# Optimization experiments

Hardware: AMD Instinct MI355X
Metric: run time of the kernel (lower is better)

Reference implementation:

```python
import jax, jax.numpy as jnp
import numpy as np

B, D_IN, D_FEAT = 256, 512, 512   # batch, encoder in-dim, encoder out-dim (= Sender input_dim)
H, V, E, L = 512, 32000, 64, 16   # hidden_size, vocab_size, embedding_dim, length


def setup_inputs() -> dict:
    key = jax.random.key(0)
    ks = jax.random.split(key, 12)
    s = lambda *d: 1.0 / np.sqrt(d[-1])
    return {
        "x": jax.random.normal(ks[0], (B, D_IN), jnp.float32),
        # encoder: Linear(D_IN, D_FEAT)
        "enc_W": jax.random.normal(ks[1], (D_FEAT, D_IN), jnp.float32) * s(D_IN),
        "enc_b": jnp.zeros((D_FEAT,), jnp.float32),
        # input_layer: Linear(D_FEAT, H)
        "in_W": jax.random.normal(ks[2], (H, D_FEAT), jnp.float32) * s(D_FEAT),
        "in_b": jnp.zeros((H,), jnp.float32),
        # GRU cell (torch layout: gates ordered r, z, n)
        "W_ih": jax.random.normal(ks[3], (3 * H, E), jnp.float32) * s(H),
        "W_hh": jax.random.normal(ks[4], (3 * H, H), jnp.float32) * s(H),
        "b_ih": jnp.zeros((3 * H,), jnp.float32),
        "b_hh": jnp.zeros((3 * H,), jnp.float32),
        # output_layer: Linear(H, V)
        "out_W": jax.random.normal(ks[5], (V, H), jnp.float32) * s(H),
        "out_b": jnp.zeros((V,), jnp.float32),
        # msg_embedding table and sos embedding parameter
        "emb_table": jax.random.normal(ks[6], (V, E), jnp.float32),
        "sos_emb": jax.random.normal(ks[7], (E,), jnp.float32),
    }


def _gru_cell(e, h, W_ih, W_hh, b_ih, b_hh):
    gi = e @ W_ih.T + b_ih            # [B, 3H]
    gh = h @ W_hh.T + b_hh            # [B, 3H]
    gi_r, gi_z, gi_n = jnp.split(gi, 3, axis=-1)
    gh_r, gh_z, gh_n = jnp.split(gh, 3, axis=-1)
    r = jax.nn.sigmoid(gi_r + gh_r)
    z = jax.nn.sigmoid(gi_z + gh_z)
    n = jnp.tanh(gi_n + r * gh_n)
    return (1.0 - z) * n + z * h


def reference(x, enc_W, enc_b, in_W, in_b, W_ih, W_hh, b_ih, b_hh,
              out_W, out_b, emb_table, sos_emb):
    # encoder -> input_layer -> initial hidden state (num_layers = 1)
    feat = x @ enc_W.T + enc_b                  # [B, D_FEAT]
    h0 = feat @ in_W.T + in_b                   # [B, H]
    e0 = jnp.broadcast_to(sos_emb, (x.shape[0], E))  # sos embedding repeated over batch

    def step(carry, _):
        h, e = carry
        h = _gru_cell(e, h, W_ih, W_hh, b_ih, b_hh)      # [B, H]
        logits_t = h @ out_W.T + out_b                    # [B, V]
        sym = jnp.argmax(logits_t, axis=-1)               # eval-mode greedy symbol [B]
        e_next = emb_table[sym]                           # [B, E]
        return (h, e_next), (sym, logits_t)

    (_, _), (syms, logits) = jax.lax.scan(step, (h0, e0), None, length=L)
    sequence = syms.T                                     # [B, L] int
    logits = jnp.transpose(logits, (1, 0, 2))             # [B, L, V]
    return sequence, logits
```

## Files before the change

### kernel.cpp

```cpp
#include <hip/hip_runtime.h>
#include <math.h>

#define BATCH 256
#define DIN 512
#define DFEAT 512
#define HSZ 512
#define VOCAB 32000
#define EMB 64
#define SLEN 16
#define NTILE 500
#define MARGIN 0.0625f

typedef __attribute__((ext_vector_type(8))) short bf16x8;
typedef __attribute__((ext_vector_type(4))) float f32x4;

__device__ inline unsigned bf16_rne(float x) {
    union { float f; unsigned u; } u; u.f = x;
    unsigned r = u.u + 0x7fff + ((u.u >> 16) & 1);
    return r >> 16;
}

template<int BM, int BN, int BK, int TM, int TN>
__global__ __launch_bounds__(256) void gemm_atb(
    const float* __restrict__ A,
    const float* __restrict__ W,
    const float* __restrict__ bias,
    float* __restrict__ C, long long ldc,
    int M, int N, int K)
{
    __shared__ float As[BK][BM + 4];
    __shared__ float Bs[BK][BN + 4];
    constexpr int THREADS = (BM / TM) * (BN / TN);
    const int tid = threadIdx.x;
    const int tx = tid % (BN / TN);
    const int ty = tid / (BN / TN);
    const int row0 = blockIdx.y * BM;
    const int col0 = blockIdx.x * BN;
    float acc[TM][TN] = {};
    for (int k0 = 0; k0 < K; k0 += BK) {
        for (int i = tid; i < BM * BK; i += THREADS) {
            int m = i / BK, k = i % BK;
            As[k][m] = A[(long long)(row0 + m) * K + k0 + k];
        }
        for (int i = tid; i < BN * BK; i += THREADS) {
            int n = i / BK, k = i % BK;
            Bs[k][n] = W[(long long)(col0 + n) * K + k0 + k];
        }
        __syncthreads();
        #pragma unroll
        for (int kk = 0; kk < BK; ++kk) {
            float a[TM], b[TN];
            #pragma unroll
            for (int i = 0; i < TM; ++i) a[i] = As[kk][ty * TM + i];
            #pragma unroll
            for (int j = 0; j < TN; ++j) b[j] = Bs[kk][tx * TN + j];
            #pragma unroll
            for (int i = 0; i < TM; ++i)
                #pragma unroll
                for (int j = 0; j < TN; ++j)
                    acc[i][j] = fmaf(a[i], b[j], acc[i][j]);
        }
        __syncthreads();
    }
    #pragma unroll
    for (int i = 0; i < TM; ++i) {
        long long m = row0 + ty * TM + i;
        float* crow = C + m * ldc;
        #pragma unroll
        for (int j = 0; j < TN; ++j) {
            int n = col0 + tx * TN + j;
            float v = acc[i][j];
            if (bias) v += bias[n];
            crow[n] = v;
        }
    }
}

__global__ void prep_kernel(const float* __restrict__ out_W, ushort* __restrict__ Wb,
                            const float* __restrict__ W_ih, const float* __restrict__ W_hh,
                            const float* __restrict__ b_ih, const float* __restrict__ b_hh,
                            float* __restrict__ Wcat2, float* __restrict__ bcat2)
{
    const int stride = gridDim.x * 256;
    const int t0 = blockIdx.x * 256 + threadIdx.x;
    for (int i = t0; i < VOCAB * HSZ / 4; i += stride) {
        const float4 v = ((const float4*)out_W)[i];
        ushort4 o;
        o.x = (ushort)bf16_rne(v.x); o.y = (ushort)bf16_rne(v.y);
        o.z = (ushort)bf16_rne(v.z); o.w = (ushort)bf16_rne(v.w);
        ((ushort4*)Wb)[i] = o;
    }
    for (long long i = t0; i < 2048LL * 576; i += stride) {
        int g = (int)(i / 576), k = (int)(i % 576);
        int j = g >> 2, comp = g & 3;
        float v;
        if (comp == 0)      v = (k < 64) ? W_ih[j * 64 + k]          : W_hh[(long long)j * 512 + k - 64];
        else if (comp == 1) v = (k < 64) ? W_ih[(512 + j) * 64 + k]  : W_hh[(long long)(512 + j) * 512 + k - 64];
        else if (comp == 2) v = (k < 64) ? W_ih[(1024 + j) * 64 + k] : 0.f;
        else                v = (k < 64) ? 0.f                        : W_hh[(long long)(1024 + j) * 512 + k - 64];
        Wcat2[i] = v;
    }
    for (int i = t0; i < 2048; i += stride) {
        int j = i >> 2, comp = i & 3;
        float bv = (comp == 0) ? b_ih[j] + b_hh[j]
                 : (comp == 1) ? b_ih[512 + j] + b_hh[512 + j]
                 : (comp == 2) ? b_ih[1024 + j] : b_hh[1024 + j];
        bcat2[i] = bv;
    }
}

template<bool FIRST>
__global__ __launch_bounds__(256) void gru_fused_kernel(
    const float* __restrict__ hprev, float* __restrict__ hnew,
    const float* __restrict__ Wcat2, const float* __restrict__ bcat2,
    const float* __restrict__ ebuf, const float* __restrict__ sos,
    ushort* __restrict__ hbf)
{
    __shared__ __align__(16) char smem[22528];
    const int tid = threadIdx.x;
    const int blk = blockIdx.x;
    const int ty = blk >> 5;
    const int tx = blk & 31;
    float* As = (float*)smem;
    float* Bs = (float*)(smem + 4608);
    const int tyt = tid >> 4;
    const int txt = tid & 15;
    float acc[4] = {};
    for (int k0 = 0; k0 < 576; k0 += 64) {
        for (int i = tid; i < 16 * 64; i += 256) {
            int m = i >> 6, k = i & 63;
            int kc = k0 + k;
            float v;
            if (kc < 64) v = FIRST ? sos[kc] : ebuf[(long long)(ty * 16 + m) * 64 + kc];
            else         v = hprev[(long long)(ty * 16 + m) * 512 + kc - 64];
            As[k * 18 + m] = v;
        }
        for (int i = tid; i < 64 * 64; i += 256) {
            int n = i >> 6, k = i & 63;
            Bs[k * 68 + n] = Wcat2[(long long)(tx * 64 + n) * 576 + k0 + k];
        }
        __syncthreads();
        #pragma unroll 8
        for (int kk = 0; kk < 64; ++kk) {
            const float a = As[kk * 18 + tyt];
            const float4 b = *(const float4*)&Bs[kk * 68 + txt * 4];
            acc[0] = fmaf(a, b.x, acc[0]);
            acc[1] = fmaf(a, b.y, acc[1]);
            acc[2] = fmaf(a, b.z, acc[2]);
            acc[3] = fmaf(a, b.w, acc[3]);
        }
        __syncthreads();
    }
    float* gt = (float*)smem;
    #pragma unroll
    for (int j = 0; j < 4; ++j)
        gt[tyt * 64 + txt * 4 + j] = acc[j];
    __syncthreads();
    {
        int row = tid >> 4, jl = tid & 15;
        int jg = tx * 16 + jl;
        float gr  = gt[row * 64 + jl * 4 + 0] + bcat2[jg * 4 + 0];
        float gz  = gt[row * 64 + jl * 4 + 1] + bcat2[jg * 4 + 1];
        float gni = gt[row * 64 + jl * 4 + 2] + bcat2[jg * 4 + 2];
        float gnh = gt[row * 64 + jl * 4 + 3] + bcat2[jg * 4 + 3];
        float r = 1.0f / (1.0f + expf(-gr));
        float z = 1.0f / (1.0f + expf(-gz));
        float n = tanhf(gni + r * gnh);
        long long bglob = ty * 16 + row;
        float hold = hprev[bglob * 512 + jg];
        float h = (1.0f - z) * n + z * hold;
        hnew[bglob * 512 + jg] = h;
        hbf[bglob * 512 + jg] = (ushort)bf16_rne(h);
    }
}

__global__ __launch_bounds__(256) void logits_bm128_kernel(
    const ushort* __restrict__ hbf,
    const ushort* __restrict__ Wb,
    const float* __restrict__ out_b,
    float* __restrict__ lbase, float* __restrict__ tmaxv)
{
    __shared__ __align__(16) char As[16384];
    __shared__ __align__(16) char Bs[8192];
    __shared__ float s_mv[128];
    const int tid = threadIdx.x;
    const int lane = tid & 63;
    const int wave = tid >> 6;
    const int bid = blockIdx.x;
    const int job = (bid & 7) * 125 + (bid >> 3);
    const int jx = job >> 1;
    const int jy = job & 1;
    const int row0 = jy * 128;
    const int col0 = jx * 64;

    f32x4 acc[2][4] = {};
    const int srow = tid >> 3;
    const int sch = tid & 7;

    for (int k0 = 0; k0 < 512; k0 += 64) {
        #pragma unroll
        for (int ra = 0; ra < 4; ++ra) {
            int row = ra * 32 + srow;
            const char* g = (const char*)(hbf + (long long)(row0 + row) * 512 + k0) + ((sch ^ (row & 7)) * 16);
            __builtin_amdgcn_global_load_lds(
                (const __attribute__((address_space(1))) void*)g,
                (__attribute__((address_space(3))) void*)(As + row * 128 + sch * 16), 16, 0, 0);
        }
        #pragma unroll
        for (int rb = 0; rb < 2; ++rb) {
            int row = rb * 32 + srow;
            const char* g = (const char*)(Wb + (long long)(col0 + row) * 512 + k0) + ((sch ^ (row & 7)) * 16);
            __builtin_amdgcn_global_load_lds(
                (const __attribute__((address_space(1))) void*)g,
                (__attribute__((address_space(3))) void*)(Bs + row * 128 + sch * 16), 16, 0, 0);
        }
        __syncthreads();
        #pragma unroll
        for (int k32 = 0; k32 < 64; k32 += 32) {
            bf16x8 af[2], bfr[4];
            #pragma unroll
            for (int f = 0; f < 2; ++f) {
                int rA = wave * 32 + f * 16 + (lane & 15);
                int byteA = (rA * 128 + (k32 + ((lane >> 4) << 3)) * 2) ^ ((rA & 7) << 4);
                af[f] = *(const bf16x8*)&As[byteA];
            }
            #pragma unroll
            for (int j = 0; j < 4; ++j) {
                int rB = j * 16 + (lane & 15);
                int byteB = (rB * 128 + (k32 + ((lane >> 4) << 3)) * 2) ^ ((rB & 7) << 4);
                bfr[j] = *(const bf16x8*)&Bs[byteB];
            }
            #pragma unroll
            for (int f = 0; f < 2; ++f)
                #pragma unroll
                for (int j = 0; j < 4; ++j)
                    acc[f][j] = __builtin_amdgcn_mfma_f32_16x16x32_bf16(af[f], bfr[j], acc[f][j], 0, 0, 0);
        }
        __syncthreads();
    }

    #pragma unroll
    for (int f = 0; f < 2; ++f) {
        #pragma unroll
        for (int q = 0; q < 4; ++q) {
            int r_local = wave * 32 + f * 16 + ((lane >> 4) << 2) + q;
            float* crow = lbase + (long long)(row0 + r_local) * (SLEN * (long long)VOCAB);
            float mv = -INFINITY;
            #pragma unroll
            for (int j = 0; j < 4; ++j) {
                int c = col0 + j * 16 + (lane & 15);
                float v = acc[f][j][q] + out_b[c];
                __builtin_nontemporal_store(v, &crow[c]);
                mv = fmaxf(mv, v);
            }
            #pragma unroll
            for (int m = 1; m < 16; m <<= 1) mv = fmaxf(mv, __shfl_xor(mv, m, 64));
            if ((lane & 15) == 0) s_mv[r_local] = mv;
        }
    }
    __syncthreads();
    if (tid < 128)
        tmaxv[(long long)(row0 + tid) * 512 + jx] = s_mv[tid];
}

__global__ __launch_bounds__(256) void argmax_kernel(
    const float* __restrict__ tmaxv, const float* __restrict__ lbase,
    const float* __restrict__ h, const float* __restrict__ out_W,
    const float* __restrict__ out_b, const float* __restrict__ emb,
    float* __restrict__ seq, float* __restrict__ ebuf, int t)
{
    __shared__ float s_red[256];
    __shared__ int s_qt[64];
    __shared__ int s_cand[64];
    __shared__ float s_rv[64];
    __shared__ int s_cnt2[2];
    __shared__ int s_sym;
    const int b = blockIdx.x;
    const int tid = threadIdx.x;
    const int lane = tid & 63, wave = tid >> 6;
    const float* row = lbase + (long long)b * (SLEN * (long long)VOCAB);

    float v0 = tmaxv[(long long)b * 512 + tid];
    float v1 = (tid + 256 < NTILE) ? tmaxv[(long long)b * 512 + 256 + tid] : -INFINITY;
    s_red[tid] = fmaxf(v0, v1); __syncthreads();
    for (int s = 128; s > 0; s >>= 1) {
        if (tid < s) s_red[tid] = fmaxf(s_red[tid], s_red[tid + s]);
        __syncthreads();
    }
    float M = s_red[0];
    if (tid == 0) { s_cnt2[0] = 0; s_cnt2[1] = 0; }
    __syncthreads();
    if (v0 >= M - MARGIN) {
        int s = atomicAdd(&s_cnt2[0], 1);
        if (s < 64) s_qt[s] = tid;
    }
    if (v1 >= M - MARGIN) {
        int s = atomicAdd(&s_cnt2[0], 1);
        if (s < 64) s_qt[s] = tid + 256;
    }
    __syncthreads();
    int nq = min(s_cnt2[0], 64);
    for (int idx = tid; idx < nq * 64; idx += 256) {
        int c = s_qt[idx >> 6] * 64 + (idx & 63);
        if (row[c] >= M - MARGIN) {
            int s = atomicAdd(&s_cnt2[1], 1);
            if (s < 64) s_cand[s] = c;
        }
    }
    __syncthreads();
    int nc = min(s_cnt2[1], 64);
    const float* hrow = h + (long long)b * 512;
    for (int ci = wave; ci < nc; ci += 4) {
        int vv = s_cand[ci];
        const float* wrow = out_W + (long long)vv * 512;
        float s = 0.f;
        for (int k = lane; k < 512; k += 64) s = fmaf(hrow[k], wrow[k], s);
        for (int off = 32; off > 0; off >>= 1) s += __shfl_down(s, off, 64);
        if (lane == 0) s_rv[ci] = s + out_b[vv];
    }
    __syncthreads();
    if (tid == 0) {
        float bv = -INFINITY; int sym = 0x7fffffff;
        for (int ci = 0; ci < nc; ++ci) {
            float xx = s_rv[ci]; int c = s_cand[ci];
            if (xx > bv || (xx == bv && c < sym)) { bv = xx; sym = c; }
        }
        if (sym < 0 || sym >= VOCAB) sym = 0;
        seq[b * SLEN + t] = (float)sym;
        s_sym = sym;
    }
    __syncthreads();
    if (tid < EMB) ebuf[(long long)b * EMB + tid] = emb[(long long)s_sym * EMB + tid];
}

extern "C" void kernel_launch(void* const* d_in, const int* in_sizes, int n_in,
                              void* d_out, int out_size, void* d_ws, size_t ws_size,
                              hipStream_t stream) {
    const float* x     = (const float*)d_in[0];
    const float* enc_W = (const float*)d_in[1];
    const float* enc_b = (const float*)d_in[2];
    const float* in_W  = (const float*)d_in[3];
    const float* in_b  = (const float*)d_in[4];
    const float* W_ih  = (const float*)d_in[5];
    const float* W_hh  = (const float*)d_in[6];
    const float* b_ih  = (const float*)d_in[7];
    const float* b_hh  = (const float*)d_in[8];
    const float* out_W = (const float*)d_in[9];
    const float* out_b = (const float*)d_in[10];
    const float* emb   = (const float*)d_in[11];
    const float* sos   = (const float*)d_in[12];

    float* seq    = (float*)d_out;
    float* logits = (float*)d_out + BATCH * SLEN;

    char* p = (char*)d_ws;
    ushort* Wb    = (ushort*)p;  p += (size_t)VOCAB * HSZ * 2;
    float* Wcat2  = (float*)p;   p += (size_t)2048 * 576 * 4;
    float* bcat2  = (float*)p;   p += 2048 * 4;
    float* hA     = (float*)p;   p += (size_t)BATCH * HSZ * 4;
    float* hB     = (float*)p;   p += (size_t)BATCH * HSZ * 4;
    ushort* hbf   = (ushort*)p;  p += (size_t)BATCH * HSZ * 2;
    float* ebuf   = (float*)p;   p += (size_t)BATCH * EMB * 4;
    float* feat   = (float*)p;   p += (size_t)BATCH * DFEAT * 4;
    float* tmaxv  = (float*)p;   p += (size_t)BATCH * 512 * 4;

    prep_kernel<<<1024, 256, 0, stream>>>(out_W, Wb, W_ih, W_hh, b_ih, b_hh, Wcat2, bcat2);
    gemm_atb<64, 64, 32, 4, 4><<<dim3(DFEAT / 64, BATCH / 64), 256, 0, stream>>>(
        x, enc_W, enc_b, feat, DFEAT, BATCH, DFEAT, DIN);
    gemm_atb<64, 64, 32, 4, 4><<<dim3(HSZ / 64, BATCH / 64), 256, 0, stream>>>(
        feat, in_W, in_b, hA, HSZ, BATCH, HSZ, DFEAT);

    float* hc = hA;
    float* hn = hB;
    for (int t = 0; t < SLEN; ++t) {
        float* lbase = logits + (long long)t * VOCAB;
        if (t == 0) {
            gru_fused_kernel<true><<<512, 256, 0, stream>>>(
                hc, hn, Wcat2, bcat2, ebuf, sos, hbf);
        } else {
            gru_fused_kernel<false><<<512, 256, 0, stream>>>(
                hc, hn, Wcat2, bcat2, ebuf, sos, hbf);
        }
        logits_bm128_kernel<<<1000, 256, 0, stream>>>(hbf, Wb, out_b, lbase, tmaxv);
        argmax_kernel<<<BATCH, 256, 0, stream>>>(
            tmaxv, lbase, hn, out_W, out_b, emb, seq, ebuf, t);
        float* tmp = hc; hc = hn; hn = tmp;
    }
}
```

Baseline: 1.230 ms.

## Fuse argmax into next GRU step with atomic counter handoff

Moves the per-step argmax and embedding lookup into the first 256 blocks of the next GRU kernel, which removes one kernel launch per step. The GRU blocks compute the hidden-state part of the gate GEMM first, then spin on a global atomic counter until all argmax blocks have published the new embeddings, and only then do the embedding part of K. This overlaps the argmax with the hidden-state GEMM. It depends on the argmax blocks making progress while other blocks spin; all 512 blocks must be co-resident, otherwise it could deadlock.

```diff
diff --git a/kernel.cpp b/kernel.cpp
--- a/kernel.cpp
+++ b/kernel.cpp
@@ -79,7 +79,8 @@
 __global__ void prep_kernel(const float* __restrict__ out_W, ushort* __restrict__ Wb,
                             const float* __restrict__ W_ih, const float* __restrict__ W_hh,
                             const float* __restrict__ b_ih, const float* __restrict__ b_hh,
-                            float* __restrict__ Wcat2, float* __restrict__ bcat2)
+                            float* __restrict__ Wcat2, float* __restrict__ bcat2,
+                            int* __restrict__ done)
 {
     const int stride = gridDim.x * 256;
     const int t0 = blockIdx.x * 256 + threadIdx.x;
@@ -107,18 +108,94 @@
                  : (comp == 2) ? b_ih[1024 + j] : b_hh[1024 + j];
         bcat2[i] = bv;
     }
+    if (t0 == 0) *done = 0;
 }
 
 template<bool FIRST>
-__global__ __launch_bounds__(256) void gru_fused_kernel(
+__global__ __launch_bounds__(256) void ag2_kernel(
     const float* __restrict__ hprev, float* __restrict__ hnew,
     const float* __restrict__ Wcat2, const float* __restrict__ bcat2,
-    const float* __restrict__ ebuf, const float* __restrict__ sos,
-    ushort* __restrict__ hbf)
+    float* __restrict__ ebuf, const float* __restrict__ sos,
+    ushort* __restrict__ hbf,
+    const float* __restrict__ tmaxv, const float* __restrict__ lprev,
+    const float* __restrict__ out_W, const float* __restrict__ out_b,
+    const float* __restrict__ emb, float* __restrict__ seq,
+    int* __restrict__ done, int wait_target, int tprev)
 {
     __shared__ __align__(16) char smem[22528];
+    __shared__ float s_red[256];
+    __shared__ int s_qt[64];
+    __shared__ int s_cand[64];
+    __shared__ float s_rv[64];
+    __shared__ int s_cnt2[2];
+    __shared__ int s_sym;
     const int tid = threadIdx.x;
+    const int lane = tid & 63, wave = tid >> 6;
     const int blk = blockIdx.x;
+
+    if (!FIRST && blk < BATCH) {
+        const int b = blk;
+        const float* row = lprev + (long long)b * (SLEN * (long long)VOCAB);
+        float v0 = tmaxv[(long long)b * 512 + tid];
+        float v1 = (tid + 256 < NTILE) ? tmaxv[(long long)b * 512 + 256 + tid] : -INFINITY;
+        s_red[tid] = fmaxf(v0, v1); __syncthreads();
+        for (int s = 128; s > 0; s >>= 1) {
+            if (tid < s) s_red[tid] = fmaxf(s_red[tid], s_red[tid + s]);
+            __syncthreads();
+        }
+        float M = s_red[0];
+        if (tid == 0) { s_cnt2[0] = 0; s_cnt2[1] = 0; }
+        __syncthreads();
+        if (v0 >= M - MARGIN) {
+            int s = atomicAdd(&s_cnt2[0], 1);
+            if (s < 64) s_qt[s] = tid;
+        }
+        if (v1 >= M - MARGIN) {
+            int s = atomicAdd(&s_cnt2[0], 1);
+            if (s < 64) s_qt[s] = tid + 256;
+        }
+        __syncthreads();
+        int nq = min(s_cnt2[0], 64);
+        for (int idx = tid; idx < nq * 64; idx += 256) {
+            int c = s_qt[idx >> 6] * 64 + (idx & 63);
+            if (row[c] >= M - MARGIN) {
+                int s = atomicAdd(&s_cnt2[1], 1);
+                if (s < 64) s_cand[s] = c;
+            }
+        }
+        __syncthreads();
+        int nc = min(s_cnt2[1], 64);
+        const float* hrow = hprev + (long long)b * 512;
+        for (int ci = wave; ci < nc; ci += 4) {
+            int vv = s_cand[ci];
+            const float* wrow = out_W + (long long)vv * 512;
+            float s = 0.f;
+            for (int k = lane; k < 512; k += 64) s = fmaf(hrow[k], wrow[k], s);
+            for (int off = 32; off > 0; off >>= 1) s += __shfl_down(s, off, 64);
+            if (lane == 0) s_rv[ci] = s + out_b[vv];
+        }
+        __syncthreads();
+        if (tid == 0) {
+            float bv = -INFINITY; int sym = 0x7fffffff;
+            for (int ci = 0; ci < nc; ++ci) {
+                float xx = s_rv[ci]; int c = s_cand[ci];
+                if (xx > bv || (xx == bv && c < sym)) { bv = xx; sym = c; }
+            }
+            if (sym < 0 || sym >= VOCAB) sym = 0;
+            seq[b * SLEN + tprev] = (float)sym;
+            s_sym = sym;
+        }
+        __syncthreads();
+        if (tid < EMB)
+            __hip_atomic_store(&ebuf[(long long)b * EMB + tid],
+                               emb[(long long)s_sym * EMB + tid],
+                               __ATOMIC_RELAXED, __HIP_MEMORY_SCOPE_AGENT);
+        __syncthreads();
+        if (tid == 0)
+            __hip_atomic_fetch_add(done, 1, __ATOMIC_RELEASE, __HIP_MEMORY_SCOPE_AGENT);
+        __syncthreads();
+    }
+
     const int ty = blk >> 5;
     const int tx = blk & 31;
     float* As = (float*)smem;
@@ -126,14 +203,11 @@
     const int tyt = tid >> 4;
     const int txt = tid & 15;
     float acc[4] = {};
-    for (int k0 = 0; k0 < 576; k0 += 64) {
+
+    for (int k0 = 64; k0 < 576; k0 += 64) {
         for (int i = tid; i < 16 * 64; i += 256) {
             int m = i >> 6, k = i & 63;
-            int kc = k0 + k;
-            float v;
-            if (kc < 64) v = FIRST ? sos[kc] : ebuf[(long long)(ty * 16 + m) * 64 + kc];
-            else         v = hprev[(long long)(ty * 16 + m) * 512 + kc - 64];
-            As[k * 18 + m] = v;
+            As[k * 18 + m] = hprev[(long long)(ty * 16 + m) * 512 + (k0 - 64) + k];
         }
         for (int i = tid; i < 64 * 64; i += 256) {
             int n = i >> 6, k = i & 63;
@@ -151,6 +225,41 @@
         }
         __syncthreads();
     }
+
+    if (!FIRST) {
+        if (tid == 0) {
+            while (__hip_atomic_load(done, __ATOMIC_RELAXED, __HIP_MEMORY_SCOPE_AGENT) < wait_target)
+                __builtin_amdgcn_s_sleep(8);
+            __hip_atomic_load(done, __ATOMIC_ACQUIRE, __HIP_MEMORY_SCOPE_AGENT);
+        }
+        __syncthreads();
+    }
+    {
+        for (int i = tid; i < 16 * 64; i += 256) {
+            int m = i >> 6, k = i & 63;
+            float v;
+            if (FIRST) v = sos[k];
+            else v = __hip_atomic_load(&ebuf[(long long)(ty * 16 + m) * EMB + k],
+                                       __ATOMIC_RELAXED, __HIP_MEMORY_SCOPE_AGENT);
+            As[k * 18 + m] = v;
+        }
+        for (int i = tid; i < 64 * 64; i += 256) {
+            int n = i >> 6, k = i & 63;
+            Bs[k * 68 + n] = Wcat2[(long long)(tx * 64 + n) * 576 + k];
+        }
+        __syncthreads();
+        #pragma unroll 8
+        for (int kk = 0; kk < 64; ++kk) {
+            const float a = As[kk * 18 + tyt];
+            const float4 b = *(const float4*)&Bs[kk * 68 + txt * 4];
+            acc[0] = fmaf(a, b.x, acc[0]);
+            acc[1] = fmaf(a, b.y, acc[1]);
+            acc[2] = fmaf(a, b.z, acc[2]);
+            acc[3] = fmaf(a, b.w, acc[3]);
+        }
+        __syncthreads();
+    }
+
     float* gt = (float*)smem;
     #pragma unroll
     for (int j = 0; j < 4; ++j)
@@ -363,8 +472,10 @@
     float* ebuf   = (float*)p;   p += (size_t)BATCH * EMB * 4;
     float* feat   = (float*)p;   p += (size_t)BATCH * DFEAT * 4;
     float* tmaxv  = (float*)p;   p += (size_t)BATCH * 512 * 4;
-
-    prep_kernel<<<1024, 256, 0, stream>>>(out_W, Wb, W_ih, W_hh, b_ih, b_hh, Wcat2, bcat2);
+    int*   done   = (int*)p;     p += 64;
+
+    prep_kernel<<<1024, 256, 0, stream>>>(out_W, Wb, W_ih, W_hh, b_ih, b_hh,
+                                          Wcat2, bcat2, done);
     gemm_atb<64, 64, 32, 4, 4><<<dim3(DFEAT / 64, BATCH / 64), 256, 0, stream>>>(
         x, enc_W, enc_b, feat, DFEAT, BATCH, DFEAT, DIN);
     gemm_atb<64, 64, 32, 4, 4><<<dim3(HSZ / 64, BATCH / 64), 256, 0, stream>>>(
@@ -375,15 +486,19 @@
     for (int t = 0; t < SLEN; ++t) {
         float* lbase = logits + (long long)t * VOCAB;
         if (t == 0) {
-            gru_fused_kernel<true><<<512, 256, 0, stream>>>(
-                hc, hn, Wcat2, bcat2, ebuf, sos, hbf);
+            ag2_kernel<true><<<512, 256, 0, stream>>>(
+                hc, hn, Wcat2, bcat2, ebuf, sos, hbf,
+                tmaxv, logits, out_W, out_b, emb, seq, done, 0, 0);
         } else {
-            gru_fused_kernel<false><<<512, 256, 0, stream>>>(
-                hc, hn, Wcat2, bcat2, ebuf, sos, hbf);
+            ag2_kernel<false><<<512, 256, 0, stream>>>(
+                hc, hn, Wcat2, bcat2, ebuf, sos, hbf,
+                tmaxv, logits + (long long)(t - 1) * VOCAB,
+                out_W, out_b, emb, seq, done, 256 * t, t - 1);
         }
         logits_bm128_kernel<<<1000, 256, 0, stream>>>(hbf, Wb, out_b, lbase, tmaxv);
-        argmax_kernel<<<BATCH, 256, 0, stream>>>(
-            tmaxv, lbase, hn, out_W, out_b, emb, seq, ebuf, t);
         float* tmp = hc; hc = hn; hn = tmp;
     }
-}
+    argmax_kernel<<<BATCH, 256, 0, stream>>>(
+        tmaxv, logits + (long long)(SLEN - 1) * VOCAB, hc, out_W, out_b, emb,
+        seq, ebuf, SLEN - 1);
+}
```

New measurement: 1.150 ms. 6.5% less time.
